# Kernel optimization log

Hardware: AMD Instinct MI355X
Metric: run time of the kernel (lower is better)

The kernel has to match this reference:

```python
import jax, jax.numpy as jnp
import numpy as np

B, N, H, O = 262144, 64, 256, 64
MAX_ITER = 30
TOL = 1e-7
NU = 1.0


def setup_inputs() -> dict:
    key = jax.random.key(0)
    kx, kr, k1, k2, k3, k4 = jax.random.split(key, 6)
    x = jax.random.normal(kx, (B, N), dtype=jnp.float32) * 3.0
    r = jax.random.uniform(kr, (N,), dtype=jnp.float32) + 0.5  # positive rates in [0.5, 1.5)
    # MLP params (torch Linear: y = x @ W.T + b), Kaiming-ish scaling
    W1 = jax.random.normal(k1, (H, N), dtype=jnp.float32) * (1.0 / np.sqrt(N))
    b1 = jax.random.normal(k2, (H,), dtype=jnp.float32) * 0.01
    W2 = jax.random.normal(k3, (O, H), dtype=jnp.float32) * (1.0 / np.sqrt(H))
    b2 = jax.random.normal(k4, (O,), dtype=jnp.float32) * 0.01
    return {"x": x, "r": r, "W1": W1, "b1": b1, "W2": W2, "b2": b2}


def _solve_s(x, r):
    """Vectorized Newton solve of sum_i e^{-2 r_i s} x_i^2 = 1 per sample.

    Replicates solve_s_single: s starts at 0, up to MAX_ITER Newton steps,
    frozen once |F(s)| < TOL; all-zero samples return s = 0.
    """
    x2 = x * x  # [B, N]
    zero_mask = jnp.all(jnp.abs(x) <= 1e-12, axis=1)  # torch.allclose(x, 0, atol=1e-12)

    def body(_, s):
        e = jnp.exp(-2.0 * r[None, :] * s[:, None])        # [B, N]
        val = jnp.sum(e * x2, axis=1) - 1.0                # F(s)     [B]
        dval = jnp.sum(-2.0 * r[None, :] * e * x2, axis=1) # F'(s)    [B]
        safe_d = jnp.where(dval == 0.0, 1.0, dval)
        step = val / safe_d
        step = jnp.where((jnp.abs(val) < TOL) | zero_mask, 0.0, step)
        return s - step

    s0 = jnp.zeros(x.shape[0], dtype=x.dtype)
    return jax.lax.fori_loop(0, MAX_ITER, body, s0)


def reference(x, r, W1, b1, W2, b2):
    S = _solve_s(x, r)[:, None]                 # [B, 1], detached in torch (built via .item())
    S = jax.lax.stop_gradient(S)
    x_sphere = x * jnp.exp(-r[None, :] * S)     # d(-s) x
    h = jnp.maximum(x_sphere @ W1.T + b1, 0.0)  # [B, H]
    mlp_out = h @ W2.T + b2                     # [B, O]
    return mlp_out * jnp.exp(NU * S)
```

## Files before the change

### kernel.cpp

```cpp
#include <hip/hip_runtime.h>

typedef __attribute__((ext_vector_type(8))) short short8;
typedef __attribute__((ext_vector_type(4))) float floatx4;

static __device__ __forceinline__ unsigned short f2bf(float f) {
    unsigned u = __float_as_uint(f);
    u += 0x7FFFu + ((u >> 16) & 1u);
    return (unsigned short)(u >> 16);
}

__global__ __launch_bounds__(512, 2) void fused_k(const float* __restrict__ x,
                                                  const float* __restrict__ r,
                                                  const float* __restrict__ W1f,
                                                  const float* __restrict__ b1,
                                                  const float* __restrict__ W2f,
                                                  const float* __restrict__ b2,
                                                  float* __restrict__ out,
                                                  int tiles_per_block) {
    __shared__ unsigned short sW1[256 * 64];
    __shared__ unsigned short sW2[64 * 256];
    __shared__ float sB1[256];

    int tid = threadIdx.x;

    const float4* w1f4 = (const float4*)W1f;
#pragma unroll
    for (int c = 0; c < 4; ++c) {
        int g = tid + c * 512;
        int h = g >> 3, ch = g & 7;
        int prow = ((h >> 5) * 2 + ((h >> 2) & 1)) * 16 + ((h >> 3) & 3) * 4 + (h & 3);
        float4 lo = w1f4[2 * g], hi = w1f4[2 * g + 1];
        uint4 p;
        p.x = (unsigned)f2bf(lo.x) | ((unsigned)f2bf(lo.y) << 16);
        p.y = (unsigned)f2bf(lo.z) | ((unsigned)f2bf(lo.w) << 16);
        p.z = (unsigned)f2bf(hi.x) | ((unsigned)f2bf(hi.y) << 16);
        p.w = (unsigned)f2bf(hi.z) | ((unsigned)f2bf(hi.w) << 16);
        *(uint4*)&sW1[prow * 64 + (ch ^ (prow & 7)) * 8] = p;
    }
    const float4* w2f4 = (const float4*)W2f;
#pragma unroll
    for (int c = 0; c < 4; ++c) {
        int g = tid + c * 512;
        float4 lo = w2f4[2 * g], hi = w2f4[2 * g + 1];
        uint4 p;
        p.x = (unsigned)f2bf(lo.x) | ((unsigned)f2bf(lo.y) << 16);
        p.y = (unsigned)f2bf(lo.z) | ((unsigned)f2bf(lo.w) << 16);
        p.z = (unsigned)f2bf(hi.x) | ((unsigned)f2bf(hi.y) << 16);
        p.w = (unsigned)f2bf(hi.z) | ((unsigned)f2bf(hi.w) << 16);
        int row = g >> 5, ch = g & 31;
        *(uint4*)&sW2[row * 256 + (ch ^ (row & 7)) * 8] = p;
    }
    if (tid < 256) {
        int h = tid;
        int prow = ((h >> 5) * 2 + ((h >> 2) & 1)) * 16 + ((h >> 3) & 3) * 4 + (h & 3);
        sB1[prow] = b1[h];
    }
    __syncthreads();

    int wave = tid >> 6, lane = tid & 63;
    int q = lane >> 4, l16 = lane & 15;
    int sx = l16 & 7;

    float bias2[4];
#pragma unroll
    for (int n = 0; n < 4; ++n) bias2[n] = b2[n * 16 + l16];

    const float L2E2 = 2.8853900817779268f;
    float rl2[16];
    {
        const float4* r4 = (const float4*)r;
        float4 ra = r4[2 * q], rb = r4[2 * q + 1];
        float4 rc = r4[8 + 2 * q], rd = r4[8 + 2 * q + 1];
        rl2[0] = ra.x * L2E2; rl2[1] = ra.y * L2E2; rl2[2] = ra.z * L2E2; rl2[3] = ra.w * L2E2;
        rl2[4] = rb.x * L2E2; rl2[5] = rb.y * L2E2; rl2[6] = rb.z * L2E2; rl2[7] = rb.w * L2E2;
        rl2[8] = rc.x * L2E2; rl2[9] = rc.y * L2E2; rl2[10] = rc.z * L2E2; rl2[11] = rc.w * L2E2;
        rl2[12] = rd.x * L2E2; rl2[13] = rd.y * L2E2; rl2[14] = rd.z * L2E2; rl2[15] = rd.w * L2E2;
    }

    for (int tt = 0; tt < tiles_per_block; ++tt) {
        size_t m0 = ((size_t)blockIdx.x * tiles_per_block + tt) * 128;
        int myrow = wave * 16 + l16;

        const float4* x4 = (const float4*)(x + (m0 + myrow) * 64);
        float4 va = x4[2 * q], vb = x4[2 * q + 1];
        float4 vc = x4[8 + 2 * q], vd = x4[8 + 2 * q + 1];
        float xv[16];
        xv[0] = va.x; xv[1] = va.y; xv[2] = va.z; xv[3] = va.w;
        xv[4] = vb.x; xv[5] = vb.y; xv[6] = vb.z; xv[7] = vb.w;
        xv[8] = vc.x; xv[9] = vc.y; xv[10] = vc.z; xv[11] = vc.w;
        xv[12] = vd.x; xv[13] = vd.y; xv[14] = vd.z; xv[15] = vd.w;

        float x2[16], rx2[16];
        float sum0 = 0.f, sumr = 0.f;
        int nz = 0;
#pragma unroll
        for (int j = 0; j < 16; ++j) {
            x2[j] = xv[j] * xv[j];
            rx2[j] = rl2[j] * x2[j];
            sum0 += x2[j];
            sumr += rx2[j];
            nz |= (fabsf(xv[j]) > 1e-12f) ? 1 : 0;
        }
        sum0 += __shfl_xor(sum0, 16); sum0 += __shfl_xor(sum0, 32);
        sumr += __shfl_xor(sumr, 16); sumr += __shfl_xor(sumr, 32);
        nz   |= __shfl_xor(nz, 16);   nz   |= __shfl_xor(nz, 32);

        float s = 0.f;
        if (nz) {
            s = __log2f(sum0) * sum0 * __builtin_amdgcn_rcpf(sumr);
#pragma unroll 1
            for (int it = 0; it < 10; ++it) {
                float ns = -s;
                float v = 0.f, dv = 0.f;
#pragma unroll
                for (int j = 0; j < 16; ++j) {
                    float e = __builtin_amdgcn_exp2f(ns * rl2[j]);
                    v = fmaf(e, x2[j], v);
                    dv = fmaf(e, rx2[j], dv);
                }
                v += __shfl_xor(v, 16);   v += __shfl_xor(v, 32);
                dv += __shfl_xor(dv, 16); dv += __shfl_xor(dv, 32);
                if (__all(fabsf(v - 1.f) < 1e-5f)) break;
                s += __log2f(v) * v * __builtin_amdgcn_rcpf(dv);
            }
        }

        float hs = -0.5f * s;
        short8 a0, a1;
#pragma unroll
        for (int j = 0; j < 8; ++j)
            a0[j] = (short)f2bf(xv[j] * __builtin_amdgcn_exp2f(hs * rl2[j]));
#pragma unroll
        for (int j = 0; j < 8; ++j)
            a1[j] = (short)f2bf(xv[8 + j] * __builtin_amdgcn_exp2f(hs * rl2[8 + j]));

        float es = __builtin_amdgcn_exp2f(s * 1.4426950408889634f);
        float sc[4];
#pragma unroll
        for (int reg = 0; reg < 4; ++reg) sc[reg] = __shfl(es, q * 4 + reg);

        floatx4 oacc[4];
#pragma unroll
        for (int n = 0; n < 4; ++n)
            oacc[n] = (floatx4){bias2[n], bias2[n], bias2[n], bias2[n]};

#pragma unroll
        for (int hc = 0; hc < 8; ++hc) {
            unsigned pk0, pk1, pk2, pk3;
            {
                int t = hc * 2;
                int row = t * 16 + l16;
                short8 wb0 = *(const short8*)&sW1[row * 64 + (q ^ sx) * 8];
                short8 wb1 = *(const short8*)&sW1[row * 64 + ((q + 4) ^ sx) * 8];
                const float4 bb = *(const float4*)&sB1[t * 16 + q * 4];
                floatx4 acc = (floatx4){bb.x, bb.y, bb.z, bb.w};
                acc = __builtin_amdgcn_mfma_f32_16x16x32_bf16(wb0, a0, acc, 0, 0, 0);
                acc = __builtin_amdgcn_mfma_f32_16x16x32_bf16(wb1, a1, acc, 0, 0, 0);
                float h0 = fmaxf(acc[0], 0.f), h1 = fmaxf(acc[1], 0.f);
                float h2 = fmaxf(acc[2], 0.f), h3 = fmaxf(acc[3], 0.f);
                asm("v_cvt_pk_bf16_f32 %0, %1, %2" : "=v"(pk0) : "v"(h0), "v"(h1));
                asm("v_cvt_pk_bf16_f32 %0, %1, %2" : "=v"(pk1) : "v"(h2), "v"(h3));
            }
            {
                int t = hc * 2 + 1;
                int row = t * 16 + l16;
                short8 wb0 = *(const short8*)&sW1[row * 64 + (q ^ sx) * 8];
                short8 wb1 = *(const short8*)&sW1[row * 64 + ((q + 4) ^ sx) * 8];
                const float4 bb = *(const float4*)&sB1[t * 16 + q * 4];
                floatx4 acc = (floatx4){bb.x, bb.y, bb.z, bb.w};
                acc = __builtin_amdgcn_mfma_f32_16x16x32_bf16(wb0, a0, acc, 0, 0, 0);
                acc = __builtin_amdgcn_mfma_f32_16x16x32_bf16(wb1, a1, acc, 0, 0, 0);
                float h0 = fmaxf(acc[0], 0.f), h1 = fmaxf(acc[1], 0.f);
                float h2 = fmaxf(acc[2], 0.f), h3 = fmaxf(acc[3], 0.f);
                asm("v_cvt_pk_bf16_f32 %0, %1, %2" : "=v"(pk2) : "v"(h0), "v"(h1));
                asm("v_cvt_pk_bf16_f32 %0, %1, %2" : "=v"(pk3) : "v"(h2), "v"(h3));
            }
            int4 hw = make_int4((int)pk0, (int)pk1, (int)pk2, (int)pk3);
            short8 ha = *(short8*)&hw;
#pragma unroll
            for (int n = 0; n < 4; ++n) {
                int orow = n * 16 + l16;
                short8 wb = *(const short8*)&sW2[orow * 256 + ((hc * 4 + q) ^ sx) * 8];
                oacc[n] = __builtin_amdgcn_mfma_f32_16x16x32_bf16(ha, wb, oacc[n], 0, 0, 0);
            }
        }
#pragma unroll
        for (int n = 0; n < 4; ++n) {
#pragma unroll
            for (int reg = 0; reg < 4; ++reg) {
                out[(m0 + wave * 16 + q * 4 + reg) * 64 + n * 16 + l16] =
                    oacc[n][reg] * sc[reg];
            }
        }
    }
}

extern "C" void kernel_launch(void* const* d_in, const int* in_sizes, int n_in,
                              void* d_out, int out_size, void* d_ws, size_t ws_size,
                              hipStream_t stream) {
    const float* x  = (const float*)d_in[0];
    const float* r  = (const float*)d_in[1];
    const float* W1 = (const float*)d_in[2];
    const float* b1 = (const float*)d_in[3];
    const float* W2 = (const float*)d_in[4];
    const float* b2 = (const float*)d_in[5];
    float* out = (float*)d_out;
    int B = in_sizes[0] / 64;

    int tiles = B / 128;
    int blocks = 512;
    int tpb = tiles / blocks;

    fused_k<<<blocks, 512, 0, stream>>>(x, r, W1, b1, W2, b2, out, tpb);
}
```

Before: 139.0 us.

## Prefetch next x tile, use Halley-style log-Newton, pack bf16 with hardware cvt

Loads the next tile's x rows into registers before computing the current tile, so global load latency overlaps with the solve. The log-domain Newton step gains a second-derivative (Halley-type) correction and the iteration cap drops from 10 to 8, aiming for fewer iterations at the cost of an extra accumulator and shuffle reduction per iteration. The bf16 conversion of the activation fragment uses the packed v_cvt_pk_bf16_f32 instruction instead of manual rounding. Risks are extra register pressure and different convergence behaviour near the tolerance.

Result: no change. 140.5 us (+1.1%).

```diff
diff --git a/kernel.cpp b/kernel.cpp
--- a/kernel.cpp
+++ b/kernel.cpp
@@ -77,26 +77,37 @@
         rl2[12] = rd.x * L2E2; rl2[13] = rd.y * L2E2; rl2[14] = rd.z * L2E2; rl2[15] = rd.w * L2E2;
     }
 
+    int myrow = wave * 16 + l16;
+    size_t mb = (size_t)blockIdx.x * tiles_per_block * 128;
+    const float4* xt = (const float4*)(x + (mb + myrow) * 64);
+
+    float4 va = xt[2 * q], vb = xt[2 * q + 1];
+    float4 vc = xt[8 + 2 * q], vd = xt[8 + 2 * q + 1];
+
     for (int tt = 0; tt < tiles_per_block; ++tt) {
-        size_t m0 = ((size_t)blockIdx.x * tiles_per_block + tt) * 128;
-        int myrow = wave * 16 + l16;
-
-        const float4* x4 = (const float4*)(x + (m0 + myrow) * 64);
-        float4 va = x4[2 * q], vb = x4[2 * q + 1];
-        float4 vc = x4[8 + 2 * q], vd = x4[8 + 2 * q + 1];
+        size_t m0 = mb + (size_t)tt * 128;
+
         float xv[16];
         xv[0] = va.x; xv[1] = va.y; xv[2] = va.z; xv[3] = va.w;
         xv[4] = vb.x; xv[5] = vb.y; xv[6] = vb.z; xv[7] = vb.w;
         xv[8] = vc.x; xv[9] = vc.y; xv[10] = vc.z; xv[11] = vc.w;
         xv[12] = vd.x; xv[13] = vd.y; xv[14] = vd.z; xv[15] = vd.w;
 
-        float x2[16], rx2[16];
+        {
+            int nt = (tt + 1 < tiles_per_block) ? (tt + 1) : tt;
+            const float4* xn = xt + (size_t)nt * 2048;
+            va = xn[2 * q]; vb = xn[2 * q + 1];
+            vc = xn[8 + 2 * q]; vd = xn[8 + 2 * q + 1];
+        }
+
+        float x2[16], rx2[16], r2x2[16];
         float sum0 = 0.f, sumr = 0.f;
         int nz = 0;
 #pragma unroll
         for (int j = 0; j < 16; ++j) {
             x2[j] = xv[j] * xv[j];
             rx2[j] = rl2[j] * x2[j];
+            r2x2[j] = rl2[j] * rx2[j];
             sum0 += x2[j];
             sumr += rx2[j];
             nz |= (fabsf(xv[j]) > 1e-12f) ? 1 : 0;
@@ -109,30 +120,40 @@
         if (nz) {
             s = __log2f(sum0) * sum0 * __builtin_amdgcn_rcpf(sumr);
 #pragma unroll 1
-            for (int it = 0; it < 10; ++it) {
+            for (int it = 0; it < 8; ++it) {
                 float ns = -s;
-                float v = 0.f, dv = 0.f;
+                float v = 0.f, dv = 0.f, d2 = 0.f;
 #pragma unroll
                 for (int j = 0; j < 16; ++j) {
                     float e = __builtin_amdgcn_exp2f(ns * rl2[j]);
-                    v = fmaf(e, x2[j], v);
+                    v  = fmaf(e, x2[j], v);
                     dv = fmaf(e, rx2[j], dv);
+                    d2 = fmaf(e, r2x2[j], d2);
                 }
-                v += __shfl_xor(v, 16);   v += __shfl_xor(v, 32);
+                v  += __shfl_xor(v, 16);  v  += __shfl_xor(v, 32);
                 dv += __shfl_xor(dv, 16); dv += __shfl_xor(dv, 32);
+                d2 += __shfl_xor(d2, 16); d2 += __shfl_xor(d2, 32);
                 if (__all(fabsf(v - 1.f) < 1e-5f)) break;
-                s += __log2f(v) * v * __builtin_amdgcn_rcpf(dv);
+                float l2v = __log2f(v);
+                float rdv = __builtin_amdgcn_rcpf(dv);
+                float tcor = (0.34657359f * l2v) * fmaf(d2 * v, rdv * rdv, -1.f);
+                tcor = fminf(tcor, 0.7f);
+                s += l2v * v * rdv * __builtin_amdgcn_rcpf(1.f - tcor);
             }
         }
 
         float hs = -0.5f * s;
-        short8 a0, a1;
-#pragma unroll
-        for (int j = 0; j < 8; ++j)
-            a0[j] = (short)f2bf(xv[j] * __builtin_amdgcn_exp2f(hs * rl2[j]));
-#pragma unroll
-        for (int j = 0; j < 8; ++j)
-            a1[j] = (short)f2bf(xv[8 + j] * __builtin_amdgcn_exp2f(hs * rl2[8 + j]));
+        unsigned pa[8];
+#pragma unroll
+        for (int j = 0; j < 8; ++j) {
+            float ea = xv[2 * j] * __builtin_amdgcn_exp2f(hs * rl2[2 * j]);
+            float eb = xv[2 * j + 1] * __builtin_amdgcn_exp2f(hs * rl2[2 * j + 1]);
+            asm("v_cvt_pk_bf16_f32 %0, %1, %2" : "=v"(pa[j]) : "v"(ea), "v"(eb));
+        }
+        int4 w0 = make_int4((int)pa[0], (int)pa[1], (int)pa[2], (int)pa[3]);
+        int4 w1 = make_int4((int)pa[4], (int)pa[5], (int)pa[6], (int)pa[7]);
+        short8 a0 = *(short8*)&w0;
+        short8 a1 = *(short8*)&w1;
 
         float es = __builtin_amdgcn_exp2f(s * 1.4426950408889634f);
         float sc[4];
```
